# Optimization experiments

Measured on AMD Instinct MI355X. Metric: run time of the kernel, lower is better.

Reference implementation:

```python
import jax, jax.numpy as jnp
import numpy as np

T, N, F, H = 64, 20000, 8, 32
E = 320000
NEG_SLOPE = 0.01  # torch.nn.LeakyReLU default


def setup_inputs() -> dict:
    key = jax.random.key(0)
    ks = jax.random.split(key, 16)
    g = lambda k, shape, fan_in: jax.random.normal(k, shape, jnp.float32) * (1.0 / np.sqrt(fan_in))
    return {
        "x": jax.random.normal(ks[0], (T, N, F), jnp.float32),
        "edge_index": jax.random.randint(ks[1], (2, E), 0, N, jnp.int64),
        "edge_weight": jax.random.uniform(ks[2], (E,), jnp.float32),
        "h": jnp.zeros((N, H), jnp.float32),
        # GConvGRU(K=1): each ChebConv reduces to a dense Linear (only T_0 = X term)
        "Wxz": g(ks[3], (F, H), F), "bxz": jnp.zeros((H,), jnp.float32),
        "Whz": g(ks[4], (H, H), H), "bhz": jnp.zeros((H,), jnp.float32),
        "Wxr": g(ks[5], (F, H), F), "bxr": jnp.zeros((H,), jnp.float32),
        "Whr": g(ks[6], (H, H), H), "bhr": jnp.zeros((H,), jnp.float32),
        "Wxh": g(ks[7], (F, H), F), "bxh": jnp.zeros((H,), jnp.float32),
        "Whh": g(ks[8], (H, H), H), "bhh": jnp.zeros((H,), jnp.float32),
        "W1": g(ks[9], (H, 1), H), "b1": jnp.zeros((1,), jnp.float32),
        "W2": g(ks[10], (N, 1), N), "b2": jnp.zeros((1,), jnp.float32),
    }


def reference(x, edge_index, edge_weight, h,
              Wxz, bxz, Whz, bhz, Wxr, bxr, Whr, bhr, Wxh, bxh, Whh, bhh,
              W1, b1, W2, b2):
    # GConvGRU with Chebyshev order K=1: each ChebConv is out = X @ W + b
    # (edge_index / edge_weight only participate for K >= 2, faithful to source).
    def gru_step(hc, xt):  # hc: [N,H], xt: [N,F]
        z = jax.nn.sigmoid(xt @ Wxz + bxz + hc @ Whz + bhz)
        r = jax.nn.sigmoid(xt @ Wxr + bxr + hc @ Whr + bhr)
        h_tilde = jnp.tanh(xt @ Wxh + bxh + (hc * r) @ Whh + bhh)
        hn = z * hc + (1.0 - z) * h_tilde
        return hn, hn

    h_fin, h_tensor = jax.lax.scan(gru_step, h, x)  # h_tensor: [T,N,H]
    a = jax.nn.leaky_relu(h_tensor, NEG_SLOPE)       # LeakyReLU(h_tensor)
    a = jax.nn.leaky_relu(a @ W1 + b1, NEG_SLOPE)    # linear1 -> [T,N,1], then LeakyReLU
    a = a[..., 0]                                    # squeeze -> [T,N]
    out = (a @ W2 + b2)[..., 0]                      # linear2 -> [T,1] -> squeeze -> [T]
    return (out, h_fin)
```

## Files before the change

### kernel.cpp

```cpp
#include <hip/hip_runtime.h>
#include <hip/hip_bf16.h>

#define T_STEPS 64
#define N_NODES 20000
#define F_IN    8
#define H_DIM   32
#define NEG_SLOPE 0.01f
#define WS_STRIDE 32
#define LOG2E 1.44269504f

typedef __attribute__((ext_vector_type(8))) short bf16x8;
typedef __attribute__((ext_vector_type(4))) float f32x4;

#define MFMA(a, b, c) __builtin_amdgcn_mfma_f32_16x16x32_bf16((a), (b), (c), 0, 0, 0)

__device__ __forceinline__ unsigned short f2bf(float f) {
    unsigned u = __float_as_uint(f);
    u += 0x7FFFu + ((u >> 16) & 1u);
    return (unsigned short)(u >> 16);
}
__device__ __forceinline__ float bf2f(unsigned short s) {
    return __uint_as_float(((unsigned)s) << 16);
}
__device__ __forceinline__ void split_pack8_rne(const float* v, bf16x8& hi, bf16x8& lo) {
    union { unsigned u[4]; bf16x8 v8; } H, L;
#pragma unroll
    for (int p = 0; p < 4; ++p) {
        float a = v[2*p], b = v[2*p+1];
        unsigned short ha = f2bf(a), hb = f2bf(b);
        unsigned short la = f2bf(a - bf2f(ha)), lb = f2bf(b - bf2f(hb));
        H.u[p] = (unsigned)ha | ((unsigned)hb << 16);
        L.u[p] = (unsigned)la | ((unsigned)lb << 16);
    }
    hi = H.v8; lo = L.v8;
}

__device__ __forceinline__ unsigned cvtpk(float a, float b) {
    union { __hip_bfloat162 h; unsigned u; } U;
    U.h = __float22bfloat162_rn(float2{a, b});
    return U.u;
}


__device__ __forceinline__ void load_wfragW(const float* __restrict__ W, int c, int q,
                                            int Rout, int Rown, int Roth, float scale,
                                            bf16x8& hi, bf16x8& lo) {
    float v[8];
#pragma unroll
    for (int j = 0; j < 8; ++j) {
        int dim = (j < 4) ? (Rown + 4*q + j) : (Roth + 4*q + (j - 4));
        v[j] = W[dim * H_DIM + (Rout + c)] * scale;
    }
    split_pack8_rne(v, hi, lo);
}

__device__ __forceinline__ bf16x8 load_xwfragW(const float* __restrict__ Wx,
                                               const float* __restrict__ bx,
                                               const float* __restrict__ bh,
                                               int c, int q, int Rout, float scale) {
    union { unsigned short s[8]; bf16x8 v8; } U;
#pragma unroll
    for (int j = 0; j < 8; ++j) U.s[j] = 0;
    if (q == 0) {
#pragma unroll
        for (int j = 0; j < 8; ++j) U.s[j] = f2bf(Wx[j * H_DIM + Rout + c] * scale);
    } else if (q == 1) {
#pragma unroll
        for (int j = 0; j < 8; ++j) {
            float w0 = Wx[j * H_DIM + Rout + c] * scale;
            unsigned short h = f2bf(w0);
            U.s[j] = f2bf(w0 - bf2f(h));
        }
    } else if (q == 3) {
        float b = (bx[Rout + c] + bh[Rout + c]) * scale;
        unsigned short h = f2bf(b);
        U.s[0] = h;
        U.s[1] = f2bf(b - bf2f(h));
    }
    return U.v8;
}

__device__ __forceinline__ bf16x8 frag4(unsigned o01, unsigned o23,
                                        unsigned p01, unsigned p23) {
    union { unsigned u[4]; bf16x8 v8; } U;
    U.u[0] = o01; U.u[1] = o23; U.u[2] = p01; U.u[3] = p23;
    return U.v8;
}

__device__ __forceinline__ float sigmoid2_f(float xp) {
    return __builtin_amdgcn_rcpf(1.0f + __builtin_amdgcn_exp2f(-xp));
}
__device__ __forceinline__ float tanh2_f(float yp) {
    return 1.0f - 2.0f * __builtin_amdgcn_rcpf(1.0f + __builtin_amdgcn_exp2f(yp));
}
__device__ __forceinline__ float leaky_f(float x) {
    return fmaxf(x, NEG_SLOPE * x);
}

__global__ void final_kernel(const float* __restrict__ ws, const float* __restrict__ b2,
                             float* __restrict__ out) {
    int t = threadIdx.x;
    if (t < T_STEPS) out[t] = ws[t * WS_STRIDE] + b2[0];
}

__global__ __launch_bounds__(128, 3) void rgcn_mfma_kernel(
    const float* __restrict__ x,
    const float* __restrict__ h0,
    const float* __restrict__ Wxz, const float* __restrict__ bxz,
    const float* __restrict__ Whz, const float* __restrict__ bhz,
    const float* __restrict__ Wxr, const float* __restrict__ bxr,
    const float* __restrict__ Whr, const float* __restrict__ bhr,
    const float* __restrict__ Wxh, const float* __restrict__ bxh,
    const float* __restrict__ Whh, const float* __restrict__ bhh,
    const float* __restrict__ W1,  const float* __restrict__ b1,
    const float* __restrict__ W2,
    float* __restrict__ ws,
    float* __restrict__ out)
{
    const int tid  = threadIdx.x;
    const int w    = tid >> 6;
    const int l    = tid & 63;
    const int c    = l & 15;
    const int q    = l >> 4;
    const int base = blockIdx.x * 16;
    const int node = base + c;
    const int Rown = 16 * w;
    const int Roth = 16 - Rown;

    __shared__ __align__(16) unsigned xbuf[T_STEPS][16][4];
    __shared__ __align__(8) uint2 hxbuf[2][2][4][16];
    __shared__ unsigned short pbuf16[T_STEPS][2][17];

    bf16x8 WHrOh, WHrOl, WHrTh, WHrTl, WHzh, WHzl, WHhh, WHhl;
    load_wfragW(Whr, c, q, Rown, Rown, Roth, LOG2E,        WHrOh, WHrOl);
    load_wfragW(Whr, c, q, Roth, Rown, Roth, LOG2E,        WHrTh, WHrTl);
    load_wfragW(Whz, c, q, Rown, Rown, Roth, LOG2E,        WHzh,  WHzl);
    load_wfragW(Whh, c, q, Rown, Rown, Roth, 2.0f * LOG2E, WHhh,  WHhl);
    bf16x8 WXrO = load_xwfragW(Wxr, bxr, bhr, c, q, Rown, LOG2E);
    bf16x8 WXrT = load_xwfragW(Wxr, bxr, bhr, c, q, Roth, LOG2E);
    bf16x8 WXz  = load_xwfragW(Wxz, bxz, bhz, c, q, Rown, LOG2E);
    bf16x8 WXh  = load_xwfragW(Wxh, bxh, bhh, c, q, Rown, 2.0f * LOG2E);

    float w1v[4];
#pragma unroll
    for (int i = 0; i < 4; ++i) w1v[i] = W1[Rown + 4*q + i];
    const float b1s = b1[0];
    const float w2l = W2[node];

    float hv[4];
    unsigned own01, own23;
    {
        float4 h4 = ((const float4*)(h0 + (size_t)node * H_DIM + Rown))[q];
        hv[0] = h4.x; hv[1] = h4.y; hv[2] = h4.z; hv[3] = h4.w;
        own01 = cvtpk(hv[0], hv[1]);
        own23 = cvtpk(hv[2], hv[3]);
        hxbuf[0][w][q][c] = uint2{own01, own23};
    }

#pragma unroll
    for (int it = 0; it < 16; ++it) {
        int idx = it * 128 + tid;
        int t   = idx >> 5;
        int ce  = (idx >> 1) & 15;
        int hf  = idx & 1;
        const float4 v = *(const float4*)(
            x + ((size_t)t * N_NODES + base + ce) * F_IN + hf * 4);
        xbuf[t][ce][hf * 2]     = cvtpk(v.x, v.y);
        xbuf[t][ce][hf * 2 + 1] = cvtpk(v.z, v.w);
    }

    const f32x4 zero4 = {0.0f, 0.0f, 0.0f, 0.0f};
    const unsigned ONES2 = 0x3F803F80u;
    const bool q3 = (q == 3);

    __syncthreads();

    f32x4 axrO, axrT, axz, axh;
    {
        uint4 X = *(const uint4*)&xbuf[0][c][0];
        bf16x8 fx0 = frag4(q3 ? ONES2 : X.x, X.y, X.z, X.w);
        axrO = MFMA(WXrO, fx0, zero4);
        axrT = MFMA(WXrT, fx0, zero4);
        axz  = MFMA(WXz,  fx0, zero4);
        axh  = MFMA(WXh,  fx0, zero4);
    }

#pragma unroll 1
    for (int t = 0; t < T_STEPS; ++t) {
        const int rp = t & 1;

        uint2 ohp = hxbuf[rp][1 - w][q][c];
        int tt = (t + 1 < T_STEPS) ? (t + 1) : (T_STEPS - 1);
        uint4 X = *(const uint4*)&xbuf[tt][c][0];

        bf16x8 fh = frag4(own01, own23, ohp.x, ohp.y);

        f32x4 arOA = MFMA(WHrOh, fh, axrO);
        f32x4 arOB = MFMA(WHrOl, fh, zero4);
        f32x4 arTA = MFMA(WHrTh, fh, axrT);
        f32x4 arTB = MFMA(WHrTl, fh, zero4);
        f32x4 az   = MFMA(WHzh,  fh, axz);
        az         = MFMA(WHzl,  fh, az);
        f32x4 arO = arOA + arOB;
        f32x4 arT = arTA + arTB;

        float ph[4];
        ph[0] = __uint_as_float(ohp.x << 16);
        ph[1] = __uint_as_float(ohp.x & 0xffff0000u);
        ph[2] = __uint_as_float(ohp.y << 16);
        ph[3] = __uint_as_float(ohp.y & 0xffff0000u);

        float rh8[8];
#pragma unroll
        for (int i = 0; i < 4; ++i) {
            rh8[i]     = sigmoid2_f(arO[i]) * hv[i];
            rh8[4 + i] = sigmoid2_f(arT[i]) * ph[i];
        }
        bf16x8 frh = frag4(cvtpk(rh8[0], rh8[1]), cvtpk(rh8[2], rh8[3]),
                           cvtpk(rh8[4], rh8[5]), cvtpk(rh8[6], rh8[7]));

        f32x4 ahA = MFMA(WHhh, frh, axh);
        f32x4 ahB = MFMA(WHhl, frh, zero4);

        bf16x8 fxn = frag4(q3 ? ONES2 : X.x, X.y, X.z, X.w);
        f32x4 nxrO = MFMA(WXrO, fxn, zero4);
        f32x4 nxrT = MFMA(WXrT, fxn, zero4);
        f32x4 nxz  = MFMA(WXz,  fxn, zero4);
        f32x4 nxh  = MFMA(WXh,  fxn, zero4);

        float zv[4];
#pragma unroll
        for (int i = 0; i < 4; ++i) zv[i] = sigmoid2_f(az[i]);

        f32x4 ah = ahA + ahB;

        float pnew = 0.0f;
#pragma unroll
        for (int i = 0; i < 4; ++i) {
            float th = tanh2_f(ah[i]);
            float hn = th + zv[i] * (hv[i] - th);
            hv[i] = hn;
            pnew = fmaf(leaky_f(hn), w1v[i], pnew);
        }
        pnew += __shfl_xor(pnew, 16);
        pnew += __shfl_xor(pnew, 32);
        if (l < 16) pbuf16[t][w][c] = (unsigned short)cvtpk(pnew, pnew);

        own01 = cvtpk(hv[0], hv[1]);
        own23 = cvtpk(hv[2], hv[3]);
        hxbuf[1 - rp][w][q][c] = uint2{own01, own23};

        axrO = nxrO; axrT = nxrT; axz = nxz; axh = nxh;

        __syncthreads();
    }

#pragma unroll
    for (int rep = 0; rep < 8; ++rep) {
        int t = w * 32 + rep * 4 + q;
        float s = bf2f(pbuf16[t][0][c]) + bf2f(pbuf16[t][1][c]);
        float a2 = leaky_f(s + b1s) * w2l;
        a2 += __shfl_xor(a2, 1); a2 += __shfl_xor(a2, 2);
        a2 += __shfl_xor(a2, 4); a2 += __shfl_xor(a2, 8);
        if (c == 0) atomicAdd(&ws[t * WS_STRIDE], a2);
    }

    *(float4*)(out + T_STEPS + (size_t)node * H_DIM + Rown + 4*q) =
        (float4){hv[0], hv[1], hv[2], hv[3]};
}

extern "C" void kernel_launch(void* const* d_in, const int* in_sizes, int n_in,
                              void* d_out, int out_size, void* d_ws, size_t ws_size,
                              hipStream_t stream) {
    const float* x    = (const float*)d_in[0];
    const float* h0   = (const float*)d_in[3];
    const float* Wxz  = (const float*)d_in[4];
    const float* bxz  = (const float*)d_in[5];
    const float* Whz  = (const float*)d_in[6];
    const float* bhz  = (const float*)d_in[7];
    const float* Wxr  = (const float*)d_in[8];
    const float* bxr  = (const float*)d_in[9];
    const float* Whr  = (const float*)d_in[10];
    const float* bhr  = (const float*)d_in[11];
    const float* Wxh  = (const float*)d_in[12];
    const float* bxh  = (const float*)d_in[13];
    const float* Whh  = (const float*)d_in[14];
    const float* bhh  = (const float*)d_in[15];
    const float* W1   = (const float*)d_in[16];
    const float* b1   = (const float*)d_in[17];
    const float* W2   = (const float*)d_in[18];
    const float* b2   = (const float*)d_in[19];
    float* out = (float*)d_out;
    float* ws  = (float*)d_ws;

    const int grid = N_NODES / 16;
    rgcn_mfma_kernel<<<grid, 128, 0, stream>>>(
        x, h0, Wxz, bxz, Whz, bhz, Wxr, bxr, Whr, bhr,
        Wxh, bxh, Whh, bhh, W1, b1, W2, ws, out);

    final_kernel<<<1, 64, 0, stream>>>(ws, b2, out);
}
```

Measured before the change: 191.6 us.

## Use single-wave blocks with full hidden state per lane, removing per-step barriers

Each block now has one 64-lane wave that handles all 32 hidden dims for 16 nodes. Weight fragments are reordered so the K dimension covers the lane's own hidden slice, which removes the LDS exchange of hidden state and the __syncthreads barrier at every timestep. The per-timestep readout reduction now runs in registers, overlapped with the next step's MFMAs, instead of going through an LDS buffer and a post-loop pass. The cost is twice the MFMAs and register pressure per wave and fewer waves per block.

Result: no change. 193.8 us (+1.1%).

```diff
diff --git a/kernel.cpp b/kernel.cpp
--- a/kernel.cpp
+++ b/kernel.cpp
@@ -41,20 +41,21 @@
     return U.u;
 }
 
-
-__device__ __forceinline__ void load_wfragW(const float* __restrict__ W, int c, int q,
-                                            int Rout, int Rown, int Roth, float scale,
+__device__ __forceinline__ int sigma_dim(int q, int j) {
+    return (j < 4) ? (4*q + j) : (16 + 4*q + (j - 4));
+}
+
+__device__ __forceinline__ void load_wfragT(const float* __restrict__ W, int c, int q,
+                                            int Rout, float scale,
                                             bf16x8& hi, bf16x8& lo) {
     float v[8];
 #pragma unroll
-    for (int j = 0; j < 8; ++j) {
-        int dim = (j < 4) ? (Rown + 4*q + j) : (Roth + 4*q + (j - 4));
-        v[j] = W[dim * H_DIM + (Rout + c)] * scale;
-    }
+    for (int j = 0; j < 8; ++j)
+        v[j] = W[sigma_dim(q, j) * H_DIM + (Rout + c)] * scale;
     split_pack8_rne(v, hi, lo);
 }
 
-__device__ __forceinline__ bf16x8 load_xwfragW(const float* __restrict__ Wx,
+__device__ __forceinline__ bf16x8 load_xwfragT(const float* __restrict__ Wx,
                                                const float* __restrict__ bx,
                                                const float* __restrict__ bh,
                                                int c, int q, int Rout, float scale) {
@@ -80,10 +81,10 @@
     return U.v8;
 }
 
-__device__ __forceinline__ bf16x8 frag4(unsigned o01, unsigned o23,
-                                        unsigned p01, unsigned p23) {
+__device__ __forceinline__ bf16x8 frag4(unsigned w0, unsigned w1,
+                                        unsigned w2, unsigned w3) {
     union { unsigned u[4]; bf16x8 v8; } U;
-    U.u[0] = o01; U.u[1] = o23; U.u[2] = p01; U.u[3] = p23;
+    U.u[0] = w0; U.u[1] = w1; U.u[2] = w2; U.u[3] = w3;
     return U.v8;
 }
 
@@ -103,7 +104,7 @@
     if (t < T_STEPS) out[t] = ws[t * WS_STRIDE] + b2[0];
 }
 
-__global__ __launch_bounds__(128, 3) void rgcn_mfma_kernel(
+__global__ __launch_bounds__(64, 2) void rgcn_mfma_kernel(
     const float* __restrict__ x,
     const float* __restrict__ h0,
     const float* __restrict__ Wxz, const float* __restrict__ bxz,
@@ -117,49 +118,51 @@
     float* __restrict__ ws,
     float* __restrict__ out)
 {
-    const int tid  = threadIdx.x;
-    const int w    = tid >> 6;
-    const int l    = tid & 63;
+    const int l    = threadIdx.x;
     const int c    = l & 15;
     const int q    = l >> 4;
     const int base = blockIdx.x * 16;
     const int node = base + c;
-    const int Rown = 16 * w;
-    const int Roth = 16 - Rown;
 
     __shared__ __align__(16) unsigned xbuf[T_STEPS][16][4];
-    __shared__ __align__(8) uint2 hxbuf[2][2][4][16];
-    __shared__ unsigned short pbuf16[T_STEPS][2][17];
-
-    bf16x8 WHrOh, WHrOl, WHrTh, WHrTl, WHzh, WHzl, WHhh, WHhl;
-    load_wfragW(Whr, c, q, Rown, Rown, Roth, LOG2E,        WHrOh, WHrOl);
-    load_wfragW(Whr, c, q, Roth, Rown, Roth, LOG2E,        WHrTh, WHrTl);
-    load_wfragW(Whz, c, q, Rown, Rown, Roth, LOG2E,        WHzh,  WHzl);
-    load_wfragW(Whh, c, q, Rown, Rown, Roth, 2.0f * LOG2E, WHhh,  WHhl);
-    bf16x8 WXrO = load_xwfragW(Wxr, bxr, bhr, c, q, Rown, LOG2E);
-    bf16x8 WXrT = load_xwfragW(Wxr, bxr, bhr, c, q, Roth, LOG2E);
-    bf16x8 WXz  = load_xwfragW(Wxz, bxz, bhz, c, q, Rown, LOG2E);
-    bf16x8 WXh  = load_xwfragW(Wxh, bxh, bhh, c, q, Rown, 2.0f * LOG2E);
-
-    float w1v[4];
-#pragma unroll
-    for (int i = 0; i < 4; ++i) w1v[i] = W1[Rown + 4*q + i];
+
+    bf16x8 WHr0h, WHr0l, WHr1h, WHr1l;
+    bf16x8 WHz0h, WHz0l, WHz1h, WHz1l;
+    bf16x8 WHh0h, WHh0l, WHh1h, WHh1l;
+    load_wfragT(Whr, c, q, 0,  LOG2E,        WHr0h, WHr0l);
+    load_wfragT(Whr, c, q, 16, LOG2E,        WHr1h, WHr1l);
+    load_wfragT(Whz, c, q, 0,  LOG2E,        WHz0h, WHz0l);
+    load_wfragT(Whz, c, q, 16, LOG2E,        WHz1h, WHz1l);
+    load_wfragT(Whh, c, q, 0,  2.0f * LOG2E, WHh0h, WHh0l);
+    load_wfragT(Whh, c, q, 16, 2.0f * LOG2E, WHh1h, WHh1l);
+    bf16x8 WXr0 = load_xwfragT(Wxr, bxr, bhr, c, q, 0,  LOG2E);
+    bf16x8 WXr1 = load_xwfragT(Wxr, bxr, bhr, c, q, 16, LOG2E);
+    bf16x8 WXz0 = load_xwfragT(Wxz, bxz, bhz, c, q, 0,  LOG2E);
+    bf16x8 WXz1 = load_xwfragT(Wxz, bxz, bhz, c, q, 16, LOG2E);
+    bf16x8 WXh0 = load_xwfragT(Wxh, bxh, bhh, c, q, 0,  2.0f * LOG2E);
+    bf16x8 WXh1 = load_xwfragT(Wxh, bxh, bhh, c, q, 16, 2.0f * LOG2E);
+
+    float w1v[8];
+#pragma unroll
+    for (int j = 0; j < 8; ++j) w1v[j] = W1[sigma_dim(q, j)];
     const float b1s = b1[0];
     const float w2l = W2[node];
 
-    float hv[4];
-    unsigned own01, own23;
+    float hv8[8];
     {
-        float4 h4 = ((const float4*)(h0 + (size_t)node * H_DIM + Rown))[q];
-        hv[0] = h4.x; hv[1] = h4.y; hv[2] = h4.z; hv[3] = h4.w;
-        own01 = cvtpk(hv[0], hv[1]);
-        own23 = cvtpk(hv[2], hv[3]);
-        hxbuf[0][w][q][c] = uint2{own01, own23};
-    }
-
-#pragma unroll
-    for (int it = 0; it < 16; ++it) {
-        int idx = it * 128 + tid;
+        const float4 ha = ((const float4*)(h0 + (size_t)node * H_DIM))[q];
+        const float4 hb = ((const float4*)(h0 + (size_t)node * H_DIM + 16))[q];
+        hv8[0] = ha.x; hv8[1] = ha.y; hv8[2] = ha.z; hv8[3] = ha.w;
+        hv8[4] = hb.x; hv8[5] = hb.y; hv8[6] = hb.z; hv8[7] = hb.w;
+    }
+    unsigned fh0 = cvtpk(hv8[0], hv8[1]);
+    unsigned fh1 = cvtpk(hv8[2], hv8[3]);
+    unsigned fh2 = cvtpk(hv8[4], hv8[5]);
+    unsigned fh3 = cvtpk(hv8[6], hv8[7]);
+
+#pragma unroll
+    for (int it = 0; it < 32; ++it) {
+        int idx = it * 64 + l;
         int t   = idx >> 5;
         int ce  = (idx >> 1) & 15;
         int hf  = idx & 1;
@@ -173,100 +176,118 @@
     const unsigned ONES2 = 0x3F803F80u;
     const bool q3 = (q == 3);
 
-    __syncthreads();
-
-    f32x4 axrO, axrT, axz, axh;
+    f32x4 axr0, axr1, axz0, axz1, axh0, axh1;
     {
         uint4 X = *(const uint4*)&xbuf[0][c][0];
         bf16x8 fx0 = frag4(q3 ? ONES2 : X.x, X.y, X.z, X.w);
-        axrO = MFMA(WXrO, fx0, zero4);
-        axrT = MFMA(WXrT, fx0, zero4);
-        axz  = MFMA(WXz,  fx0, zero4);
-        axh  = MFMA(WXh,  fx0, zero4);
-    }
+        axr0 = MFMA(WXr0, fx0, zero4);
+        axr1 = MFMA(WXr1, fx0, zero4);
+        axz0 = MFMA(WXz0, fx0, zero4);
+        axz1 = MFMA(WXz1, fx0, zero4);
+        axh0 = MFMA(WXh0, fx0, zero4);
+        axh1 = MFMA(WXh1, fx0, zero4);
+    }
+
+    float pls  = 0.0f;
+    float pout = 0.0f;
 
 #pragma unroll 1
     for (int t = 0; t < T_STEPS; ++t) {
-        const int rp = t & 1;
-
-        uint2 ohp = hxbuf[rp][1 - w][q][c];
+        bf16x8 fh = frag4(fh0, fh1, fh2, fh3);
+
+        f32x4 ar0A = MFMA(WHr0h, fh, axr0);
+        f32x4 ar0B = MFMA(WHr0l, fh, zero4);
+        f32x4 ar1A = MFMA(WHr1h, fh, axr1);
+        f32x4 ar1B = MFMA(WHr1l, fh, zero4);
+        f32x4 az0  = MFMA(WHz0h, fh, axz0);
+        az0        = MFMA(WHz0l, fh, az0);
+        f32x4 az1  = MFMA(WHz1h, fh, axz1);
+        az1        = MFMA(WHz1l, fh, az1);
+
         int tt = (t + 1 < T_STEPS) ? (t + 1) : (T_STEPS - 1);
         uint4 X = *(const uint4*)&xbuf[tt][c][0];
 
-        bf16x8 fh = frag4(own01, own23, ohp.x, ohp.y);
-
-        f32x4 arOA = MFMA(WHrOh, fh, axrO);
-        f32x4 arOB = MFMA(WHrOl, fh, zero4);
-        f32x4 arTA = MFMA(WHrTh, fh, axrT);
-        f32x4 arTB = MFMA(WHrTl, fh, zero4);
-        f32x4 az   = MFMA(WHzh,  fh, axz);
-        az         = MFMA(WHzl,  fh, az);
-        f32x4 arO = arOA + arOB;
-        f32x4 arT = arTA + arTB;
-
-        float ph[4];
-        ph[0] = __uint_as_float(ohp.x << 16);
-        ph[1] = __uint_as_float(ohp.x & 0xffff0000u);
-        ph[2] = __uint_as_float(ohp.y << 16);
-        ph[3] = __uint_as_float(ohp.y & 0xffff0000u);
+        if (t > 0) {
+            float s = pls;
+            s += __shfl_xor(s, 16);
+            s += __shfl_xor(s, 32);
+            float a2 = leaky_f(s + b1s) * w2l;
+            a2 += __shfl_xor(a2, 1); a2 += __shfl_xor(a2, 2);
+            a2 += __shfl_xor(a2, 4); a2 += __shfl_xor(a2, 8);
+            pout = (l == t - 1) ? a2 : pout;
+        }
+
+        f32x4 ar0 = ar0A + ar0B;
+        f32x4 ar1 = ar1A + ar1B;
 
         float rh8[8];
 #pragma unroll
         for (int i = 0; i < 4; ++i) {
-            rh8[i]     = sigmoid2_f(arO[i]) * hv[i];
-            rh8[4 + i] = sigmoid2_f(arT[i]) * ph[i];
+            rh8[i]     = sigmoid2_f(ar0[i]) * hv8[i];
+            rh8[4 + i] = sigmoid2_f(ar1[i]) * hv8[4 + i];
         }
         bf16x8 frh = frag4(cvtpk(rh8[0], rh8[1]), cvtpk(rh8[2], rh8[3]),
                            cvtpk(rh8[4], rh8[5]), cvtpk(rh8[6], rh8[7]));
 
-        f32x4 ahA = MFMA(WHhh, frh, axh);
-        f32x4 ahB = MFMA(WHhl, frh, zero4);
+        f32x4 ah0A = MFMA(WHh0h, frh, axh0);
+        f32x4 ah0B = MFMA(WHh0l, frh, zero4);
+        f32x4 ah1A = MFMA(WHh1h, frh, axh1);
+        f32x4 ah1B = MFMA(WHh1l, frh, zero4);
 
         bf16x8 fxn = frag4(q3 ? ONES2 : X.x, X.y, X.z, X.w);
-        f32x4 nxrO = MFMA(WXrO, fxn, zero4);
-        f32x4 nxrT = MFMA(WXrT, fxn, zero4);
-        f32x4 nxz  = MFMA(WXz,  fxn, zero4);
-        f32x4 nxh  = MFMA(WXh,  fxn, zero4);
-
-        float zv[4];
-#pragma unroll
-        for (int i = 0; i < 4; ++i) zv[i] = sigmoid2_f(az[i]);
-
-        f32x4 ah = ahA + ahB;
+        axr0 = MFMA(WXr0, fxn, zero4);
+        axr1 = MFMA(WXr1, fxn, zero4);
+        axz0 = MFMA(WXz0, fxn, zero4);
+        axz1 = MFMA(WXz1, fxn, zero4);
+        axh0 = MFMA(WXh0, fxn, zero4);
+        axh1 = MFMA(WXh1, fxn, zero4);
+
+        float zv[8];
+#pragma unroll
+        for (int i = 0; i < 4; ++i) {
+            zv[i]     = sigmoid2_f(az0[i]);
+            zv[4 + i] = sigmoid2_f(az1[i]);
+        }
+
+        f32x4 ah0 = ah0A + ah0B;
+        f32x4 ah1 = ah1A + ah1B;
 
         float pnew = 0.0f;
 #pragma unroll
         for (int i = 0; i < 4; ++i) {
-            float th = tanh2_f(ah[i]);
-            float hn = th + zv[i] * (hv[i] - th);
-            hv[i] = hn;
-            pnew = fmaf(leaky_f(hn), w1v[i], pnew);
-        }
-        pnew += __shfl_xor(pnew, 16);
-        pnew += __shfl_xor(pnew, 32);
-        if (l < 16) pbuf16[t][w][c] = (unsigned short)cvtpk(pnew, pnew);
-
-        own01 = cvtpk(hv[0], hv[1]);
-        own23 = cvtpk(hv[2], hv[3]);
-        hxbuf[1 - rp][w][q][c] = uint2{own01, own23};
-
-        axrO = nxrO; axrT = nxrT; axz = nxz; axh = nxh;
-
-        __syncthreads();
-    }
-
-#pragma unroll
-    for (int rep = 0; rep < 8; ++rep) {
-        int t = w * 32 + rep * 4 + q;
-        float s = bf2f(pbuf16[t][0][c]) + bf2f(pbuf16[t][1][c]);
+            float th0 = tanh2_f(ah0[i]);
+            float hn0 = th0 + zv[i] * (hv8[i] - th0);
+            hv8[i] = hn0;
+            pnew = fmaf(leaky_f(hn0), w1v[i], pnew);
+
+            float th1 = tanh2_f(ah1[i]);
+            float hn1 = th1 + zv[4 + i] * (hv8[4 + i] - th1);
+            hv8[4 + i] = hn1;
+            pnew = fmaf(leaky_f(hn1), w1v[4 + i], pnew);
+        }
+        pls = pnew;
+
+        fh0 = cvtpk(hv8[0], hv8[1]);
+        fh1 = cvtpk(hv8[2], hv8[3]);
+        fh2 = cvtpk(hv8[4], hv8[5]);
+        fh3 = cvtpk(hv8[6], hv8[7]);
+    }
+
+    {
+        float s = pls;
+        s += __shfl_xor(s, 16);
+        s += __shfl_xor(s, 32);
         float a2 = leaky_f(s + b1s) * w2l;
         a2 += __shfl_xor(a2, 1); a2 += __shfl_xor(a2, 2);
         a2 += __shfl_xor(a2, 4); a2 += __shfl_xor(a2, 8);
-        if (c == 0) atomicAdd(&ws[t * WS_STRIDE], a2);
-    }
-
-    *(float4*)(out + T_STEPS + (size_t)node * H_DIM + Rown + 4*q) =
-        (float4){hv[0], hv[1], hv[2], hv[3]};
+        pout = (l == T_STEPS - 1) ? a2 : pout;
+    }
+
+    atomicAdd(&ws[l * WS_STRIDE], pout);
+
+    float* op = out + T_STEPS + (size_t)node * H_DIM;
+    *(float4*)(op + 4 * q)      = (float4){hv8[0], hv8[1], hv8[2], hv8[3]};
+    *(float4*)(op + 16 + 4 * q) = (float4){hv8[4], hv8[5], hv8[6], hv8[7]};
 }
 
 extern "C" void kernel_launch(void* const* d_in, const int* in_sizes, int n_in,
@@ -294,7 +315,7 @@
     float* ws  = (float*)d_ws;
 
     const int grid = N_NODES / 16;
-    rgcn_mfma_kernel<<<grid, 128, 0, stream>>>(
+    rgcn_mfma_kernel<<<grid, 64, 0, stream>>>(
         x, h0, Wxz, bxz, Whz, bhz, Wxr, bxr, Whr, bhr,
         Wxh, bxh, Whh, bhh, W1, b1, W2, ws, out);
 
```
